# Kernel tuning notes

Measured on AMD Instinct MI355X. Metric: run time of the kernel, lower is better.

Reference implementation:

```python
import jax, jax.numpy as jnp
import numpy as np

NX, NY = 8192, 8192
FX, FY = 1024, 1024
EMB, EMB_OUT = 512, 512


def setup_inputs() -> dict:
    key = jax.random.key(0)
    ks = jax.random.split(key, 8)
    s = lambda f: 1.0 / np.sqrt(f)
    return {
        "x": jax.random.normal(ks[0], (NX, FX), jnp.float32),
        "y": jax.random.normal(ks[1], (NY, FY), jnp.float32),
        "Wx": jax.random.uniform(ks[2], (FX, EMB), jnp.float32, -s(FX), s(FX)),
        "bx": jax.random.uniform(ks[3], (EMB,), jnp.float32, -s(FX), s(FX)),
        "Wy": jax.random.uniform(ks[4], (FY, EMB), jnp.float32, -s(FY), s(FY)),
        "by": jax.random.uniform(ks[5], (EMB,), jnp.float32, -s(FY), s(FY)),
        "Wg": jax.random.uniform(ks[6], (EMB, EMB_OUT), jnp.float32, -s(EMB), s(EMB)),
        "bg": jax.random.uniform(ks[7], (EMB_OUT,), jnp.float32, -s(EMB), s(EMB)),
    }


def reference(x, y, Wx, bx, Wy, by, Wg, bg):
    # Linear projections: [Nx, emb], [Ny, emb]
    xp = x @ Wx + bx
    yp = y @ Wy + by
    # Pairwise affinity (Dice-coefficient style normalization)
    A_ = xp @ yp.T                              # [Nx, Ny]
    Dcol = jnp.sum(xp * xp, axis=1)[:, None]    # ||x_i||^2, diag of xp@xp.T
    Drow = jnp.sum(yp * yp, axis=1)[None, :]    # ||y_j||^2, diag of yp@yp.T
    A = 2.0 * A_ / (Dcol + Drow)                # [Nx, Ny]
    # Weighted aggregation over x nodes, then ReLU MLP
    gwf = A.T @ xp                              # [Ny, emb]
    return jax.nn.relu(gwf @ Wg + bg)           # [Ny, emb_out]
```

## Files before the change

### kernel.cpp

```cpp
#include <hip/hip_runtime.h>
#include <hip/hip_bf16.h>


typedef __attribute__((ext_vector_type(8))) short bf16x8;
typedef __attribute__((ext_vector_type(4))) short bf16x4;
typedef __attribute__((ext_vector_type(4))) float f32x4;

__device__ __forceinline__ short f2b(float f) {
    unsigned int u = __builtin_bit_cast(unsigned int, f);
    unsigned int r = (u + 0x7fffu + ((u >> 16) & 1u)) >> 16;
    return (short)r;
}
__device__ __forceinline__ float b2f(short s) {
    unsigned int u = ((unsigned int)(unsigned short)s) << 16;
    return __builtin_bit_cast(float, u);
}

__device__ __forceinline__ void cp16(const void* g, void* l) {
    __builtin_amdgcn_global_load_lds(
        (const __attribute__((address_space(1))) void*)g,
        (__attribute__((address_space(3))) void*)l, 16, 0, 0);
}

constexpr int EPI_XP  = 0;
constexpr int EPI_AT  = 1;
constexpr int EPI_BF  = 2;
constexpr int EPI_OUT = 3;

constexpr int ASRC_F32  = 0;
constexpr int ASRC_BF16 = 1;
constexpr int ASRC_SUM2 = 2;

template<int EPI, int ASRC, int TM>
__device__ __forceinline__ void gemm_core(
    const void* __restrict__ Aptr, const void* __restrict__ Aptr2, int lda,
    const short* __restrict__ Bt, int ldb,
    int N, int K, int bm, int bn, int kbase,
    const float* __restrict__ bias,
    short* __restrict__ outb, float* __restrict__ outf,
    float* __restrict__ Dacc,
    const float* __restrict__ Drow, const float* __restrict__ Dcol)
{
    constexpr int FRM = TM / 32;
    __shared__ __align__(16) short As[TM * 32];
    __shared__ __align__(16) short Bs[128 * 32];

    const int tid  = threadIdx.x;
    const int wave = tid >> 6;
    const int lane = tid & 63;
    const int quad = lane >> 4;
    const int l15  = lane & 15;
    const int wm   = (wave >> 1) * (FRM * 16);
    const int wn   = (wave & 1) * 64;

    f32x4 acc[FRM][4];
#pragma unroll
    for (int i = 0; i < FRM; i++)
#pragma unroll
        for (int j = 0; j < 4; j++)
            acc[i][j] = f32x4{0.f, 0.f, 0.f, 0.f};

    for (int k0 = 0; k0 < K; k0 += 32) {
        const int kk = kbase + k0;
        if (ASRC == ASRC_F32) {
            const float* Af = (const float*)Aptr;
#pragma unroll
            for (int s = 0; s < TM * 8 / 256; s++) {
                int seg = tid + 256 * s;
                int row = seg >> 3, c4 = seg & 7;
                const float4 v = *(const float4*)&Af[(size_t)(bm + row) * lda + kk + c4 * 4];
                bf16x4 b;
                b[0] = f2b(v.x); b[1] = f2b(v.y); b[2] = f2b(v.z); b[3] = f2b(v.w);
                *(bf16x4*)&As[row * 32 + c4 * 4] = b;
            }
        } else if (ASRC == ASRC_BF16) {
            const short* Ab = (const short*)Aptr;
#pragma unroll
            for (int s = 0; s < TM / 64; s++) {
                int seg = tid + 256 * s;
                int row = seg >> 2, c8 = seg & 3;
                cp16(&Ab[(size_t)(bm + row) * lda + kk + c8 * 8], &As[seg * 8]);
            }
        } else {
            const short* A0 = (const short*)Aptr;
            const short* A1 = (const short*)Aptr2;
#pragma unroll
            for (int s = 0; s < TM / 64; s++) {
                int seg = tid + 256 * s;
                int row = seg >> 2, c8 = seg & 3;
                const size_t off = (size_t)(bm + row) * lda + kk + c8 * 8;
                bf16x8 a0 = *(const bf16x8*)&A0[off];
                bf16x8 a1 = *(const bf16x8*)&A1[off];
                bf16x8 o;
#pragma unroll
                for (int e = 0; e < 8; e++) o[e] = f2b(b2f(a0[e]) + b2f(a1[e]));
                *(bf16x8*)&As[seg * 8] = o;
            }
        }
#pragma unroll
        for (int s = 0; s < 2; s++) {
            int seg = tid + 256 * s;
            int row = seg >> 2, c8 = seg & 3;
            cp16(&Bt[(size_t)(bn + row) * ldb + kk + c8 * 8], &Bs[seg * 8]);
        }
        __syncthreads();

        bf16x8 af[FRM], bfr[4];
#pragma unroll
        for (int i = 0; i < FRM; i++)
            af[i] = *(const bf16x8*)&As[(wm + i * 16 + l15) * 32 + quad * 8];
#pragma unroll
        for (int j = 0; j < 4; j++)
            bfr[j] = *(const bf16x8*)&Bs[(wn + j * 16 + l15) * 32 + quad * 8];
#pragma unroll
        for (int i = 0; i < FRM; i++)
#pragma unroll
            for (int j = 0; j < 4; j++)
                acc[i][j] = __builtin_amdgcn_mfma_f32_16x16x32_bf16(af[i], bfr[j], acc[i][j], 0, 0, 0);
        __syncthreads();
    }

#pragma unroll
    for (int im = 0; im < FRM; im++) {
#pragma unroll
        for (int r = 0; r < 4; r++) {
            const int gm = bm + wm + im * 16 + quad * 4 + r;
            if (EPI == EPI_XP) {
                float s = 0.f;
#pragma unroll
                for (int jn = 0; jn < 4; jn++) {
                    const int gn = bn + wn + jn * 16 + l15;
                    float v = acc[im][jn][r] + bias[gn];
                    outb[(size_t)gm * N + gn] = f2b(v);
                    s += v * v;
                }
#pragma unroll
                for (int m = 1; m < 16; m <<= 1) s += __shfl_xor(s, m, 64);
                if (l15 == 0) atomicAdd(&Dacc[gm], s);
            } else if (EPI == EPI_AT) {
                const float dy = Drow[gm];
#pragma unroll
                for (int jn = 0; jn < 4; jn++) {
                    const int gn = bn + wn + jn * 16 + l15;
                    float v = 2.f * acc[im][jn][r] / (Dcol[gn] + dy);
                    outb[(size_t)gm * N + gn] = f2b(v);
                }
            } else if (EPI == EPI_BF) {
#pragma unroll
                for (int jn = 0; jn < 4; jn++) {
                    const int gn = bn + wn + jn * 16 + l15;
                    outb[(size_t)gm * N + gn] = f2b(acc[im][jn][r]);
                }
            } else {
#pragma unroll
                for (int jn = 0; jn < 4; jn++) {
                    const int gn = bn + wn + jn * 16 + l15;
                    float v = acc[im][jn][r] + bias[gn];
                    outf[(size_t)gm * N + gn] = fmaxf(v, 0.f);
                }
            }
        }
    }
}

__global__ __launch_bounds__(256)
void k_proj(const float* __restrict__ A, const short* __restrict__ Bt,
            const float* __restrict__ bias, short* __restrict__ outb,
            float* __restrict__ Dacc)
{
    gemm_core<EPI_XP, ASRC_F32, 64>(A, nullptr, 1024, Bt, 1024, 512, 1024,
                                    blockIdx.y * 64, blockIdx.x * 128, 0,
                                    bias, outb, nullptr, Dacc, nullptr, nullptr);
}

__global__ __launch_bounds__(256)
void k_aff(const short* __restrict__ ypb, const short* __restrict__ xpb,
           short* __restrict__ At, const float* __restrict__ Dy,
           const float* __restrict__ Dx)
{
    const int flat = blockIdx.x;
    const int x  = flat & 7;
    const int q  = flat >> 3;
    const int st = q >> 6;
    const int w  = q & 63;
    const int s  = x * 8 + st;
    const int bx = (s & 7) * 8 + (w & 7);
    const int by = (s >> 3) * 8 + (w >> 3);
    gemm_core<EPI_AT, ASRC_BF16, 128>(ypb, nullptr, 512, xpb, 512, 8192, 512,
                                      by * 128, bx * 128, 0,
                                      nullptr, At, nullptr, nullptr, Dy, Dx);
}

__global__ __launch_bounds__(256)
void k_agg(const short* __restrict__ At, const short* __restrict__ xpT,
           short* __restrict__ p0, short* __restrict__ p1)
{
    const int flat = blockIdx.x;
    const int x = flat & 7;
    const int q = flat >> 3;
    const int g = x * 16 + (q >> 2);
    const int z = g >> 6;
    const int bm = (g & 63) * 128;
    const int bn = (q & 3) * 128;
    short* outb = z ? p1 : p0;
    gemm_core<EPI_BF, ASRC_BF16, 128>(At, nullptr, 8192, xpT, 8192, 512, 4096,
                                      bm, bn, z * 4096,
                                      nullptr, outb, nullptr, nullptr, nullptr, nullptr);
}

__global__ __launch_bounds__(256)
void k_out(const short* __restrict__ p0, const short* __restrict__ p1,
           const short* __restrict__ WgT, const float* __restrict__ bg,
           float* __restrict__ out)
{
    gemm_core<EPI_OUT, ASRC_SUM2, 64>(p0, p1, 512, WgT, 512, 512, 512,
                                      blockIdx.y * 64, blockIdx.x * 128, 0,
                                      bg, nullptr, out, nullptr, nullptr, nullptr);
}

__global__ __launch_bounds__(256)
void transpose_f32_bf16(const float* __restrict__ in, short* __restrict__ out, int R, int C)
{
    __shared__ short t[32][33];
    const int tx = threadIdx.x, ty = threadIdx.y;
    const int bx = blockIdx.x * 32, by = blockIdx.y * 32;
#pragma unroll
    for (int i = 0; i < 32; i += 8)
        t[ty + i][tx] = f2b(in[(size_t)(by + ty + i) * C + bx + tx]);
    __syncthreads();
#pragma unroll
    for (int i = 0; i < 32; i += 8)
        out[(size_t)(bx + ty + i) * R + by + tx] = t[tx][ty + i];
}

__global__ __launch_bounds__(256)
void transpose_bf16(const short* __restrict__ in, short* __restrict__ out, int R, int C)
{
    __shared__ short t[32][33];
    const int tx = threadIdx.x, ty = threadIdx.y;
    const int bx = blockIdx.x * 32, by = blockIdx.y * 32;
#pragma unroll
    for (int i = 0; i < 32; i += 8)
        t[ty + i][tx] = in[(size_t)(by + ty + i) * C + bx + tx];
    __syncthreads();
#pragma unroll
    for (int i = 0; i < 32; i += 8)
        out[(size_t)(bx + ty + i) * R + by + tx] = t[tx][ty + i];
}

extern "C" void kernel_launch(void* const* d_in, const int* in_sizes, int n_in,
                              void* d_out, int out_size, void* d_ws, size_t ws_size,
                              hipStream_t stream)
{
    const float* x  = (const float*)d_in[0];
    const float* y  = (const float*)d_in[1];
    const float* Wx = (const float*)d_in[2];
    const float* bx = (const float*)d_in[3];
    const float* Wy = (const float*)d_in[4];
    const float* by = (const float*)d_in[5];
    const float* Wg = (const float*)d_in[6];
    const float* bg = (const float*)d_in[7];
    float* out = (float*)d_out;

    char* p = (char*)d_ws;
    short* At   = (short*)p; p += (size_t)8192 * 8192 * 2;
    short* xpb  = (short*)p; p += (size_t)8192 * 512 * 2;
    short* ypb  = (short*)p; p += (size_t)8192 * 512 * 2;
    short* xpT  = (short*)p; p += (size_t)512 * 8192 * 2;
    short* WxT  = (short*)p; p += (size_t)512 * 1024 * 2;
    short* WyT  = (short*)p; p += (size_t)512 * 1024 * 2;
    short* WgT  = (short*)p; p += (size_t)512 * 512 * 2;
    float* Dx   = (float*)p; p += (size_t)8192 * 4;
    float* Dy   = (float*)p; p += (size_t)8192 * 4;
    short* p0 = xpb;
    short* p1 = ypb;

    hipMemsetAsync(Dx, 0, 2 * 8192 * sizeof(float), stream);

    dim3 tb(32, 8);
    transpose_f32_bf16<<<dim3(512 / 32, 1024 / 32), tb, 0, stream>>>(Wx, WxT, 1024, 512);
    transpose_f32_bf16<<<dim3(512 / 32, 1024 / 32), tb, 0, stream>>>(Wy, WyT, 1024, 512);
    transpose_f32_bf16<<<dim3(512 / 32, 512 / 32),  tb, 0, stream>>>(Wg, WgT, 512, 512);

    k_proj<<<dim3(4, 128), 256, 0, stream>>>(x, WxT, bx, xpb, Dx);
    k_proj<<<dim3(4, 128), 256, 0, stream>>>(y, WyT, by, ypb, Dy);

    transpose_bf16<<<dim3(512 / 32, 8192 / 32), tb, 0, stream>>>(xpb, xpT, 8192, 512);

    k_aff<<<4096, 256, 0, stream>>>(ypb, xpb, At, Dy, Dx);

    k_agg<<<512, 256, 0, stream>>>(At, xpT, p0, p1);

    k_out<<<dim3(4, 128), 256, 0, stream>>>(p0, p1, WgT, bg, out);
}
```

Before: 391.7 us.

## Reassociate aggregation with Wg and fuse ReLU into the aggregation GEMM

Uses associativity, (A^T xp) Wg = A^T (xp Wg), to precompute zT = (xp Wg)^T with a small GEMM. The aggregation GEMM then writes the final ReLU output directly, which removes the split-K partial buffers, the separate output GEMM and the xp transpose. The x and y inputs are converted to bf16 up front so the projection GEMMs use async LDS loads, and those bf16 copies reuse the At workspace region. This adds one bf16 rounding of xp·Wg before aggregation, and k_agg now runs the full K=8192 with 64-wide N tiles and no split-K.

Result: no change. 396.4 us (+1.2%).

```diff
diff --git a/kernel.cpp b/kernel.cpp
--- a/kernel.cpp
+++ b/kernel.cpp
@@ -11,10 +11,6 @@
     unsigned int r = (u + 0x7fffu + ((u >> 16) & 1u)) >> 16;
     return (short)r;
 }
-__device__ __forceinline__ float b2f(short s) {
-    unsigned int u = ((unsigned int)(unsigned short)s) << 16;
-    return __builtin_bit_cast(float, u);
-}
 
 __device__ __forceinline__ void cp16(const void* g, void* l) {
     __builtin_amdgcn_global_load_lds(
@@ -22,140 +18,105 @@
         (__attribute__((address_space(3))) void*)l, 16, 0, 0);
 }
 
-constexpr int EPI_XP  = 0;
-constexpr int EPI_AT  = 1;
-constexpr int EPI_BF  = 2;
-constexpr int EPI_OUT = 3;
-
-constexpr int ASRC_F32  = 0;
-constexpr int ASRC_BF16 = 1;
-constexpr int ASRC_SUM2 = 2;
-
-template<int EPI, int ASRC, int TM>
+constexpr int EPI_XP   = 0;
+constexpr int EPI_BF   = 1;
+constexpr int EPI_AT   = 2;
+constexpr int EPI_RELU = 3;
+
+template<int EPI, int TM, int TN>
 __device__ __forceinline__ void gemm_core(
-    const void* __restrict__ Aptr, const void* __restrict__ Aptr2, int lda,
+    const short* __restrict__ A, int lda,
     const short* __restrict__ Bt, int ldb,
-    int N, int K, int bm, int bn, int kbase,
+    int N, int K, int bm, int bn,
     const float* __restrict__ bias,
     short* __restrict__ outb, float* __restrict__ outf,
     float* __restrict__ Dacc,
     const float* __restrict__ Drow, const float* __restrict__ Dcol)
 {
-    constexpr int FRM = TM / 32;
+    constexpr int FRM = (TN == 128) ? (TM / 32) : 2;
     __shared__ __align__(16) short As[TM * 32];
-    __shared__ __align__(16) short Bs[128 * 32];
+    __shared__ __align__(16) short Bs[TN * 32];
 
     const int tid  = threadIdx.x;
     const int wave = tid >> 6;
     const int lane = tid & 63;
     const int quad = lane >> 4;
     const int l15  = lane & 15;
-    const int wm   = (wave >> 1) * (FRM * 16);
-    const int wn   = (wave & 1) * 64;
+    const int wn   = (TN == 128) ? (wave & 1) * 64 : 0;
+    const int wm   = (TN == 128) ? (wave >> 1) * (FRM * 16) : wave * 32;
 
     f32x4 acc[FRM][4];
 #pragma unroll
     for (int i = 0; i < FRM; i++)
 #pragma unroll
-        for (int j = 0; j < 4; j++)
-            acc[i][j] = f32x4{0.f, 0.f, 0.f, 0.f};
+        for (int j = 0; j < 4; j++) acc[i][j] = f32x4{0.f, 0.f, 0.f, 0.f};
 
     for (int k0 = 0; k0 < K; k0 += 32) {
-        const int kk = kbase + k0;
-        if (ASRC == ASRC_F32) {
-            const float* Af = (const float*)Aptr;
-#pragma unroll
-            for (int s = 0; s < TM * 8 / 256; s++) {
-                int seg = tid + 256 * s;
-                int row = seg >> 3, c4 = seg & 7;
-                const float4 v = *(const float4*)&Af[(size_t)(bm + row) * lda + kk + c4 * 4];
-                bf16x4 b;
-                b[0] = f2b(v.x); b[1] = f2b(v.y); b[2] = f2b(v.z); b[3] = f2b(v.w);
-                *(bf16x4*)&As[row * 32 + c4 * 4] = b;
-            }
-        } else if (ASRC == ASRC_BF16) {
-            const short* Ab = (const short*)Aptr;
-#pragma unroll
-            for (int s = 0; s < TM / 64; s++) {
-                int seg = tid + 256 * s;
-                int row = seg >> 2, c8 = seg & 3;
-                cp16(&Ab[(size_t)(bm + row) * lda + kk + c8 * 8], &As[seg * 8]);
-            }
-        } else {
-            const short* A0 = (const short*)Aptr;
-            const short* A1 = (const short*)Aptr2;
-#pragma unroll
-            for (int s = 0; s < TM / 64; s++) {
-                int seg = tid + 256 * s;
-                int row = seg >> 2, c8 = seg & 3;
-                const size_t off = (size_t)(bm + row) * lda + kk + c8 * 8;
-                bf16x8 a0 = *(const bf16x8*)&A0[off];
-                bf16x8 a1 = *(const bf16x8*)&A1[off];
-                bf16x8 o;
-#pragma unroll
-                for (int e = 0; e < 8; e++) o[e] = f2b(b2f(a0[e]) + b2f(a1[e]));
-                *(bf16x8*)&As[seg * 8] = o;
-            }
+#pragma unroll
+        for (int s = 0; s < TM / 64; s++) {
+            const int seg = tid + 256 * s;
+            const int row = seg >> 2, c8 = seg & 3;
+            cp16(&A[(size_t)(bm + row) * lda + k0 + c8 * 8], &As[seg * 8]);
         }
 #pragma unroll
-        for (int s = 0; s < 2; s++) {
-            int seg = tid + 256 * s;
-            int row = seg >> 2, c8 = seg & 3;
-            cp16(&Bt[(size_t)(bn + row) * ldb + kk + c8 * 8], &Bs[seg * 8]);
+        for (int s = 0; s < TN / 64; s++) {
+            const int seg = tid + 256 * s;
+            const int row = seg >> 2, c8 = seg & 3;
+            cp16(&Bt[(size_t)(bn + row) * ldb + k0 + c8 * 8], &Bs[seg * 8]);
         }
         __syncthreads();
 
-        bf16x8 af[FRM], bfr[4];
+        bf16x8 a[FRM], b[4];
 #pragma unroll
         for (int i = 0; i < FRM; i++)
-            af[i] = *(const bf16x8*)&As[(wm + i * 16 + l15) * 32 + quad * 8];
+            a[i] = *(const bf16x8*)&As[(wm + i * 16 + l15) * 32 + quad * 8];
 #pragma unroll
         for (int j = 0; j < 4; j++)
-            bfr[j] = *(const bf16x8*)&Bs[(wn + j * 16 + l15) * 32 + quad * 8];
+            b[j] = *(const bf16x8*)&Bs[(wn + j * 16 + l15) * 32 + quad * 8];
 #pragma unroll
         for (int i = 0; i < FRM; i++)
 #pragma unroll
             for (int j = 0; j < 4; j++)
-                acc[i][j] = __builtin_amdgcn_mfma_f32_16x16x32_bf16(af[i], bfr[j], acc[i][j], 0, 0, 0);
+                acc[i][j] = __builtin_amdgcn_mfma_f32_16x16x32_bf16(a[i], b[j], acc[i][j], 0, 0, 0);
         __syncthreads();
     }
 
 #pragma unroll
-    for (int im = 0; im < FRM; im++) {
-#pragma unroll
-        for (int r = 0; r < 4; r++) {
+    for (int im = 0; im < FRM; ++im) {
+#pragma unroll
+        for (int r = 0; r < 4; ++r) {
             const int gm = bm + wm + im * 16 + quad * 4 + r;
             if (EPI == EPI_XP) {
                 float s = 0.f;
 #pragma unroll
-                for (int jn = 0; jn < 4; jn++) {
-                    const int gn = bn + wn + jn * 16 + l15;
-                    float v = acc[im][jn][r] + bias[gn];
+                for (int jn = 0; jn < 4; ++jn) {
+                    const int gn = bn + wn + jn * 16 + l15;
+                    const float v = acc[im][jn][r] + bias[gn];
                     outb[(size_t)gm * N + gn] = f2b(v);
                     s += v * v;
                 }
 #pragma unroll
                 for (int m = 1; m < 16; m <<= 1) s += __shfl_xor(s, m, 64);
                 if (l15 == 0) atomicAdd(&Dacc[gm], s);
+            } else if (EPI == EPI_BF) {
+#pragma unroll
+                for (int jn = 0; jn < 4; ++jn) {
+                    const int gn = bn + wn + jn * 16 + l15;
+                    outb[(size_t)gm * N + gn] = f2b(acc[im][jn][r]);
+                }
             } else if (EPI == EPI_AT) {
                 const float dy = Drow[gm];
 #pragma unroll
-                for (int jn = 0; jn < 4; jn++) {
-                    const int gn = bn + wn + jn * 16 + l15;
-                    float v = 2.f * acc[im][jn][r] / (Dcol[gn] + dy);
+                for (int jn = 0; jn < 4; ++jn) {
+                    const int gn = bn + wn + jn * 16 + l15;
+                    const float v = 2.f * acc[im][jn][r] / (Dcol[gn] + dy);
                     outb[(size_t)gm * N + gn] = f2b(v);
                 }
-            } else if (EPI == EPI_BF) {
-#pragma unroll
-                for (int jn = 0; jn < 4; jn++) {
-                    const int gn = bn + wn + jn * 16 + l15;
-                    outb[(size_t)gm * N + gn] = f2b(acc[im][jn][r]);
-                }
             } else {
 #pragma unroll
-                for (int jn = 0; jn < 4; jn++) {
-                    const int gn = bn + wn + jn * 16 + l15;
-                    float v = acc[im][jn][r] + bias[gn];
+                for (int jn = 0; jn < 4; ++jn) {
+                    const int gn = bn + wn + jn * 16 + l15;
+                    const float v = acc[im][jn][r] + bias[gn];
                     outf[(size_t)gm * N + gn] = fmaxf(v, 0.f);
                 }
             }
@@ -164,13 +125,22 @@
 }
 
 __global__ __launch_bounds__(256)
-void k_proj(const float* __restrict__ A, const short* __restrict__ Bt,
+void k_proj(const short* __restrict__ A, const short* __restrict__ Bt,
             const float* __restrict__ bias, short* __restrict__ outb,
             float* __restrict__ Dacc)
 {
-    gemm_core<EPI_XP, ASRC_F32, 64>(A, nullptr, 1024, Bt, 1024, 512, 1024,
-                                    blockIdx.y * 64, blockIdx.x * 128, 0,
-                                    bias, outb, nullptr, Dacc, nullptr, nullptr);
+    gemm_core<EPI_XP, 64, 128>(A, 1024, Bt, 1024, 512, 1024,
+                               blockIdx.y * 64, blockIdx.x * 128,
+                               bias, outb, nullptr, Dacc, nullptr, nullptr);
+}
+
+__global__ __launch_bounds__(256)
+void k_zT(const short* __restrict__ WgT, const short* __restrict__ xpb,
+          short* __restrict__ zT)
+{
+    gemm_core<EPI_BF, 64, 128>(WgT, 512, xpb, 512, 8192, 512,
+                               blockIdx.y * 64, blockIdx.x * 128,
+                               nullptr, zT, nullptr, nullptr, nullptr, nullptr);
 }
 
 __global__ __launch_bounds__(256)
@@ -186,36 +156,33 @@
     const int s  = x * 8 + st;
     const int bx = (s & 7) * 8 + (w & 7);
     const int by = (s >> 3) * 8 + (w >> 3);
-    gemm_core<EPI_AT, ASRC_BF16, 128>(ypb, nullptr, 512, xpb, 512, 8192, 512,
-                                      by * 128, bx * 128, 0,
-                                      nullptr, At, nullptr, nullptr, Dy, Dx);
-}
-
-__global__ __launch_bounds__(256)
-void k_agg(const short* __restrict__ At, const short* __restrict__ xpT,
-           short* __restrict__ p0, short* __restrict__ p1)
+    gemm_core<EPI_AT, 128, 128>(ypb, 512, xpb, 512, 8192, 512,
+                                by * 128, bx * 128,
+                                nullptr, At, nullptr, nullptr, Dy, Dx);
+}
+
+__global__ __launch_bounds__(256)
+void k_agg(const short* __restrict__ At, const short* __restrict__ zT,
+           const float* __restrict__ bg, float* __restrict__ out)
 {
     const int flat = blockIdx.x;
-    const int x = flat & 7;
-    const int q = flat >> 3;
-    const int g = x * 16 + (q >> 2);
-    const int z = g >> 6;
-    const int bm = (g & 63) * 128;
-    const int bn = (q & 3) * 128;
-    short* outb = z ? p1 : p0;
-    gemm_core<EPI_BF, ASRC_BF16, 128>(At, nullptr, 8192, xpT, 8192, 512, 4096,
-                                      bm, bn, z * 4096,
-                                      nullptr, outb, nullptr, nullptr, nullptr, nullptr);
-}
-
-__global__ __launch_bounds__(256)
-void k_out(const short* __restrict__ p0, const short* __restrict__ p1,
-           const short* __restrict__ WgT, const float* __restrict__ bg,
-           float* __restrict__ out)
-{
-    gemm_core<EPI_OUT, ASRC_SUM2, 64>(p0, p1, 512, WgT, 512, 512, 512,
-                                      blockIdx.y * 64, blockIdx.x * 128, 0,
-                                      bg, nullptr, out, nullptr, nullptr, nullptr);
+    const int xcd = flat & 7;
+    const int q   = flat >> 3;
+    const int bm  = (xcd * 8 + (q >> 3)) * 128;
+    const int bn  = (q & 7) * 64;
+    gemm_core<EPI_RELU, 128, 64>(At, 8192, zT, 8192, 512, 8192,
+                                 bm, bn,
+                                 bg, nullptr, out, nullptr, nullptr, nullptr);
+}
+
+__global__ __launch_bounds__(256)
+void k_cvt(const float* __restrict__ in, short* __restrict__ out)
+{
+    const int i = (blockIdx.x * 256 + threadIdx.x) * 4;
+    const float4 v = *(const float4*)&in[i];
+    bf16x4 b;
+    b[0] = f2b(v.x); b[1] = f2b(v.y); b[2] = f2b(v.z); b[3] = f2b(v.w);
+    *(bf16x4*)&out[i] = b;
 }
 
 __global__ __launch_bounds__(256)
@@ -227,21 +194,6 @@
 #pragma unroll
     for (int i = 0; i < 32; i += 8)
         t[ty + i][tx] = f2b(in[(size_t)(by + ty + i) * C + bx + tx]);
-    __syncthreads();
-#pragma unroll
-    for (int i = 0; i < 32; i += 8)
-        out[(size_t)(bx + ty + i) * R + by + tx] = t[tx][ty + i];
-}
-
-__global__ __launch_bounds__(256)
-void transpose_bf16(const short* __restrict__ in, short* __restrict__ out, int R, int C)
-{
-    __shared__ short t[32][33];
-    const int tx = threadIdx.x, ty = threadIdx.y;
-    const int bx = blockIdx.x * 32, by = blockIdx.y * 32;
-#pragma unroll
-    for (int i = 0; i < 32; i += 8)
-        t[ty + i][tx] = in[(size_t)(by + ty + i) * C + bx + tx];
     __syncthreads();
 #pragma unroll
     for (int i = 0; i < 32; i += 8)
@@ -263,17 +215,18 @@
     float* out = (float*)d_out;
 
     char* p = (char*)d_ws;
-    short* At   = (short*)p; p += (size_t)8192 * 8192 * 2;
+    short* At   = (short*)p;
+    short* xb   = (short*)p;
+    short* yb   = (short*)(p + (size_t)8192 * 1024 * 2);
+    p += (size_t)8192 * 8192 * 2;
     short* xpb  = (short*)p; p += (size_t)8192 * 512 * 2;
     short* ypb  = (short*)p; p += (size_t)8192 * 512 * 2;
-    short* xpT  = (short*)p; p += (size_t)512 * 8192 * 2;
+    short* zT   = (short*)p; p += (size_t)512 * 8192 * 2;
     short* WxT  = (short*)p; p += (size_t)512 * 1024 * 2;
     short* WyT  = (short*)p; p += (size_t)512 * 1024 * 2;
     short* WgT  = (short*)p; p += (size_t)512 * 512 * 2;
     float* Dx   = (float*)p; p += (size_t)8192 * 4;
     float* Dy   = (float*)p; p += (size_t)8192 * 4;
-    short* p0 = xpb;
-    short* p1 = ypb;
 
     hipMemsetAsync(Dx, 0, 2 * 8192 * sizeof(float), stream);
 
@@ -282,14 +235,15 @@
     transpose_f32_bf16<<<dim3(512 / 32, 1024 / 32), tb, 0, stream>>>(Wy, WyT, 1024, 512);
     transpose_f32_bf16<<<dim3(512 / 32, 512 / 32),  tb, 0, stream>>>(Wg, WgT, 512, 512);
 
-    k_proj<<<dim3(4, 128), 256, 0, stream>>>(x, WxT, bx, xpb, Dx);
-    k_proj<<<dim3(4, 128), 256, 0, stream>>>(y, WyT, by, ypb, Dy);
-
-    transpose_bf16<<<dim3(512 / 32, 8192 / 32), tb, 0, stream>>>(xpb, xpT, 8192, 512);
+    k_cvt<<<8192, 256, 0, stream>>>(x, xb);
+    k_cvt<<<8192, 256, 0, stream>>>(y, yb);
+
+    k_proj<<<dim3(4, 128), 256, 0, stream>>>(xb, WxT, bx, xpb, Dx);
+    k_proj<<<dim3(4, 128), 256, 0, stream>>>(yb, WyT, by, ypb, Dy);
+
+    k_zT<<<dim3(64, 8), 256, 0, stream>>>(WgT, xpb, zT);
 
     k_aff<<<4096, 256, 0, stream>>>(ypb, xpb, At, Dy, Dx);
 
-    k_agg<<<512, 256, 0, stream>>>(At, xpT, p0, p1);
-
-    k_out<<<dim3(4, 128), 256, 0, stream>>>(p0, p1, WgT, bg, out);
-}
+    k_agg<<<512, 256, 0, stream>>>(At, zT, bg, out);
+}
```
